# Optimization experiments

Measured on AMD Instinct MI355X. Metric: run time of the kernel, lower is better.

## Reference

```python
import jax, jax.numpy as jnp
import numpy as np
import itertools

VOXEL_SIZE = np.array([0.05, 0.05, 0.1], np.float32)   # xyz, from cfg.voxel_size
GRID_OFFSET = np.array([0.0, -40.0, -3.0], np.float32)  # xyz, cfg.grid_bounds[:3]
BN_EPS = 1e-3

# ---------------- rulebook construction (numpy, mirrors spconv indice pairs) ----------------

def _enc(c, shape):
    Z, Y, X = shape
    c = c.astype(np.int64)
    return ((c[:, 0] * Z + c[:, 1]) * Y + c[:, 2]) * X + c[:, 3]

def _lookup(sk, order, q):
    pos = np.clip(np.searchsorted(sk, q), 0, len(sk) - 1)
    return np.where((q >= 0) & (sk[pos] == q), order[pos], -1).astype(np.int32)

def _subm_rulebook(coords, shape):
    # submanifold conv k=3, pad=1: output sites == input sites; neighbor = out + (k-1)
    keys = _enc(coords, shape)
    order = np.argsort(keys).astype(np.int32)
    sk = keys[order]
    dims = np.array(shape)
    rows = []
    for off in itertools.product((-1, 0, 1), repeat=3):
        nb = coords[:, 1:] + np.array(off)
        inb = ((nb >= 0) & (nb < dims)).all(1)
        full = np.concatenate([coords[:, :1], nb], 1)
        q = np.where(inb, _enc(full, shape), -1)
        rows.append(_lookup(sk, order, q))
    return np.stack(rows)  # [27, N] input index or -1

def _strided_rulebook(coords, shape_in, ksize, stride, pad):
    # regular sparse conv: out active = any site receiving a contribution; in = out*s - p + k
    ksize = np.array(ksize); stride = np.array(stride); pad = np.array(pad)
    shape_out = tuple((((np.array(shape_in) + 2 * pad - ksize) // stride) + 1).tolist())
    keys = _enc(coords, shape_in)
    order = np.argsort(keys).astype(np.int32)
    sk = keys[order]
    cand = []
    for k in itertools.product(*[range(int(x)) for x in ksize]):
        num = coords[:, 1:] + pad - np.array(k)
        ok = (num % stride == 0).all(1)
        o = num // stride
        ok &= (o >= 0).all(1) & (o < np.array(shape_out)).all(1)
        cand.append(np.concatenate([coords[ok, :1], o[ok]], 1))
    out_coords = np.unique(np.concatenate(cand, 0), axis=0).astype(np.int32)
    dims_in = np.array(shape_in)
    rows = []
    for k in itertools.product(*[range(int(x)) for x in ksize]):
        ic = out_coords[:, 1:] * stride - pad + np.array(k)
        inb = ((ic >= 0) & (ic < dims_in)).all(1)
        full = np.concatenate([out_coords[:, :1], ic], 1)
        q = np.where(inb, _enc(full, shape_in), -1)
        rows.append(_lookup(sk, order, q))
    return out_coords, np.stack(rows), shape_out

# ---------------- inputs ----------------

def setup_inputs() -> dict:
    rng = np.random.default_rng(0)
    B, NPB = 2, 8000
    shape0 = (41, 1600, 1280)
    parts = []
    for b in range(B):
        c = np.stack([rng.integers(0, shape0[0], 4 * NPB),
                      rng.integers(0, shape0[1], 4 * NPB),
                      rng.integers(0, shape0[2], 4 * NPB)], 1)
        c = np.unique(c, axis=0)[:NPB]
        parts.append(np.concatenate([np.full((len(c), 1), b), c], 1))
    coords0 = np.concatenate(parts, 0).astype(np.int32)

    rb0 = _subm_rulebook(coords0, shape0)
    coords1, rbc1, shape1 = _strided_rulebook(coords0, shape0, (3, 3, 3), (2, 2, 2), (1, 1, 1))
    rb1 = _subm_rulebook(coords1, shape1)
    coords2, rbc2, shape2 = _strided_rulebook(coords1, shape1, (3, 3, 3), (2, 2, 2), (1, 1, 1))
    rb2 = _subm_rulebook(coords2, shape2)
    coords3, rbc3, shape3 = _strided_rulebook(coords2, shape2, (3, 3, 3), (2, 2, 2), (0, 1, 1))
    rb3 = _subm_rulebook(coords3, shape3)
    coords4, rbc4, shape4 = _strided_rulebook(coords3, shape3, (3, 1, 1), (2, 1, 1), (0, 0, 0))

    def w(*s):
        return jnp.asarray((rng.standard_normal(s) * 0.1).astype(np.float32))

    inp = {"features": jnp.asarray(rng.standard_normal((len(coords0), 4)).astype(np.float32))}
    specs = [("1a", 27, 4, 16), ("1b", 27, 16, 16), ("1c", 27, 16, 32),
             ("2a", 27, 32, 32), ("2b", 27, 32, 32), ("2c", 27, 32, 64),
             ("3a", 27, 64, 64), ("3b", 27, 64, 64), ("3c", 27, 64, 64), ("3d", 27, 64, 64),
             ("4a", 27, 64, 64), ("4b", 27, 64, 64), ("4c", 27, 64, 64), ("4d", 3, 64, 64)]
    for name, K, ci, co in specs:
        inp["w" + name] = w(K, ci, co)
        inp["g" + name] = jnp.asarray((np.abs(rng.standard_normal(co)) + 0.5).astype(np.float32))
        inp["b" + name] = jnp.asarray((rng.standard_normal(co) * 0.1).astype(np.float32))
    inp.update(coordinates=jnp.asarray(coords0), coords1=jnp.asarray(coords1),
               coords2=jnp.asarray(coords2), coords3=jnp.asarray(coords3),
               rb0=jnp.asarray(rb0), rbc1=jnp.asarray(rbc1), rb1=jnp.asarray(rb1),
               rbc2=jnp.asarray(rbc2), rb2=jnp.asarray(rb2), rbc3=jnp.asarray(rbc3),
               rb3=jnp.asarray(rb3), rbc4=jnp.asarray(rbc4), batch_size=B)
    return inp

# ---------------- forward math ----------------

def _sconv(feat, rb, W):
    # gather-GEMM-scatter: rb[k,n] = input row feeding output n via kernel offset k (-1 = none)
    out = jnp.zeros((rb.shape[1], W.shape[2]), feat.dtype)
    for k in range(W.shape[0]):
        idx = rb[k]
        g = jnp.where(idx[:, None] >= 0, feat[jnp.clip(idx, 0)], 0.0)
        out = out + g @ W[k]
    return out

def _bn_relu(x, g, b):
    # BatchNorm1d in training mode over active voxels (biased var), eps=1e-3, then ReLU
    m = jnp.mean(x, 0)
    v = jnp.mean(jnp.square(x - m), 0)
    return jax.nn.relu((x - m) * (g / jnp.sqrt(v + BN_EPS)) + b)

def reference(features, w1a, g1a, b1a, w1b, g1b, b1b, w1c, g1c, b1c,
              w2a, g2a, b2a, w2b, g2b, b2b, w2c, g2c, b2c,
              w3a, g3a, b3a, w3b, g3b, b3b, w3c, g3c, b3c, w3d, g3d, b3d,
              w4a, g4a, b4a, w4b, g4b, b4b, w4c, g4c, b4c, w4d, g4d, b4d,
              coordinates, coords1, coords2, coords3,
              rb0, rbc1, rb1, rbc2, rb2, rbc3, rb3, rbc4, batch_size):
    f0 = features
    h = _bn_relu(_sconv(f0, rb0, w1a), g1a, b1a)
    h = _bn_relu(_sconv(h, rb0, w1b), g1b, b1b)
    f1 = _bn_relu(_sconv(h, rbc1, w1c), g1c, b1c)
    h = _bn_relu(_sconv(f1, rb1, w2a), g2a, b2a)
    h = _bn_relu(_sconv(h, rb1, w2b), g2b, b2b)
    f2 = _bn_relu(_sconv(h, rbc2, w2c), g2c, b2c)
    h = _bn_relu(_sconv(f2, rb2, w3a), g3a, b3a)
    h = _bn_relu(_sconv(h, rb2, w3b), g3b, b3b)
    h = _bn_relu(_sconv(h, rb2, w3c), g3c, b3c)
    f3 = _bn_relu(_sconv(h, rbc3, w3d), g3d, b3d)
    h = _bn_relu(_sconv(f3, rb3, w4a), g4a, b4a)
    h = _bn_relu(_sconv(h, rb3, w4b), g4b, b4b)
    h = _bn_relu(_sconv(h, rb3, w4c), g4c, b4c)
    f4 = _bn_relu(_sconv(h, rbc4, w4d), g4d, b4d)

    vs = jnp.asarray(VOXEL_SIZE)
    off = jnp.asarray(GRID_OFFSET)
    def to_global(stride, c):
        # indices are (b,z,y,x); flip -> (x,y,z,b); take xyz
        return jnp.flip(c, 1)[:, :3].astype(jnp.float32) * (vs * stride) + off
    xyz0 = to_global(1, coordinates)
    xyz1 = to_global(2, coords1)
    xyz2 = to_global(4, coords2)
    xyz3 = to_global(8, coords3)
    return (xyz0, f0, xyz1, f1, xyz2, f2, xyz3, f3, f4)
```

## Files before the change

### kernel.cpp

```cpp
#include <hip/hip_runtime.h>

#define BN_EPS 1e-3f
#define NREP 16

typedef __attribute__((ext_vector_type(8))) short short8;
typedef __attribute__((ext_vector_type(4))) float float4v;

__device__ __forceinline__ short f2bf(float f) {
    unsigned u = __float_as_uint(f);
    unsigned r = (u + 0x7FFFu + ((u >> 16) & 1u)) >> 16;
    return (short)r;
}

template <int N>
__device__ __forceinline__ void waitcnt_vm() {
    __builtin_amdgcn_s_waitcnt(0xF70 | (N & 15) | ((N >> 4) << 14));
}

__device__ __forceinline__ void wave_barrier() { asm volatile("s_barrier" ::: "memory"); }

__device__ __forceinline__ void dma16(const short* g, short* l) {
    __builtin_amdgcn_global_load_lds((const __attribute__((address_space(1))) void*)g,
                                     (__attribute__((address_space(3))) void*)l, 16, 0, 0);
}


__global__ __launch_bounds__(256) void zero_kernel(float* p, int n) {
    int i = blockIdx.x * 256 + threadIdx.x;
    if (i < n) p[i] = 0.f;
}

__global__ __launch_bounds__(256) void copy_kernel(const float* __restrict__ in,
                                                   float* __restrict__ out, int n) {
    int i = blockIdx.x * 256 + threadIdx.x;
    if (i < n) out[i] = in[i];
}

__global__ __launch_bounds__(256) void zero_rows_kernel(short* a, short* b, long maxN) {
    int t = threadIdx.x;
    if (t < 32) a[maxN * 32 + t] = 0;
    else if (t < 96) a[maxN * 64 + (t - 32)] = 0;
    else if (t < 128) b[maxN * 32 + (t - 96)] = 0;
    else if (t < 192) b[maxN * 64 + (t - 128)] = 0;
}

__global__ __launch_bounds__(256) void xyz_kernel(const int* __restrict__ coords,
                                                  float* __restrict__ out, int N,
                                                  float sx, float sy, float sz) {
    int n = blockIdx.x * 256 + threadIdx.x;
    if (n >= N) return;
    int4 c = ((const int4*)coords)[n];
    out[n * 3 + 0] = c.w * sx;
    out[n * 3 + 1] = c.z * sy - 40.0f;
    out[n * 3 + 2] = c.y * sz - 3.0f;
}

__global__ __launch_bounds__(256) void convert_f0(const float* __restrict__ f,
                                                  short* __restrict__ dst, int N) {
    int i = blockIdx.x * 256 + threadIdx.x;
    if (i >= N * 32) return;
    int c = i & 31, n = i >> 5;
    dst[i] = (c < 4) ? f2bf(f[n * 4 + c]) : (short)0;
}

struct PrepAll {
    const float* src[14];
    short* dst[14];
    int CI[14];
    int CO[14];
    int CHP[14];
    int cum[15];
};

__global__ __launch_bounds__(256) void prep_all_kernel(PrepAll d) {
    int i = blockIdx.x * 256 + threadIdx.x;
    if (i >= d.cum[14]) return;
    int l = 0;
    while (l < 13 && i >= d.cum[l + 1]) ++l;
    int f = i - d.cum[l];
    int CO = d.CO[l], CI = d.CI[l];
    int NCH = d.CHP[l] / 32, CT = CO / 16;
    int e = f & 7;
    int u = f >> 3;
    int l16 = u & 15;
    int q = (u >> 4) & 3;
    int u2 = u >> 6;
    int t = u2 % CT;
    int c = (u2 / CT) % NCH;
    int k = u2 / (CT * NCH);
    int ci = c * 32 + q * 8 + e;
    int co = t * 16 + l16;
    float v = (ci < CI) ? d.src[l][((size_t)k * CI + ci) * CO + co] : 0.f;
    d.dst[l][f] = f2bf(v);
}

struct ASet {
    short8 v0, v1, v2, v3;
};

template <int CHP, int CO, int K>
__global__ __launch_bounds__(512, 4) void sconv_hyb(const short* __restrict__ feat,
                                                    const int* __restrict__ rb,
                                                    const short* __restrict__ Wt,
                                                    float* __restrict__ out,
                                                    float* __restrict__ stats, int N, int zrow) {
    constexpr int NCH = CHP / 32;
    constexpr int CT = CO / 16;
    constexpr int BTILE = CO * CHP;
    constexpr int NB = BTILE / 512;
    constexpr int A = 2 * NCH;
    constexpr int ROWS = 256;
    constexpr int WAVES = 8;
    constexpr int B0 = NB / WAVES;
    constexpr int BR = NB % WAVES;

    __shared__ __align__(16) short ldsB[3 * BTILE];
    __shared__ int sIdx[K * ROWS];
    __shared__ int sFlag[K];
    __shared__ int sKl[K];
    __shared__ int sKn;

    const int tid = threadIdx.x;
    const int w = tid >> 6;
    const int lane = tid & 63;
    const int quad = lane >> 4;
    const int l16 = lane & 15;
    const int m0 = blockIdx.x * ROWS;

    if (tid < K) sFlag[tid] = 0;
    __syncthreads();
    for (int e = tid; e < K * ROWS; e += 512) {
        int r = m0 + (e & (ROWS - 1));
        int v = (r < N) ? __builtin_nontemporal_load(&rb[(size_t)(e >> 8) * N + r]) : -1;
        sIdx[e] = v;
        if (v >= 0) sFlag[e >> 8] = 1;
    }
    __syncthreads();
    if (w == 0) {
        int f = (lane < K) ? sFlag[lane] : 0;
        unsigned long long m = __ballot(f != 0);
        if (f) sKl[__popcll(m & ((1ull << lane) - 1ull))] = lane;
        if (lane == 0) sKn = (int)__popcll(m);
    }
    __syncthreads();
    const int nk = sKn;

    const short* fquad = feat + quad * 8;

    auto issueB = [&](int kp, int slot) {
        const short* wk = Wt + (size_t)kp * BTILE + lane * 8;
        short* bb = ldsB + slot * BTILE;
#pragma unroll
        for (int jj = 0; jj < (NB + WAVES - 1) / WAVES; ++jj) {
            int j = jj * WAVES + w;
            if (j < NB) dma16(wk + j * 512, bb + j * 512);
        }
    };
    auto issueA = [&](int kp) {
        ASet s;
        int i0 = sIdx[kp * ROWS + w * 32 + l16];
        int i1 = sIdx[kp * ROWS + w * 32 + 16 + l16];
        const short* p0 = fquad + (size_t)(i0 < 0 ? zrow : i0) * CHP;
        const short* p1 = fquad + (size_t)(i1 < 0 ? zrow : i1) * CHP;
        s.v0 = *(const short8*)p0;
        s.v2 = *(const short8*)p1;
        if constexpr (NCH == 2) {
            s.v1 = *(const short8*)(p0 + 32);
            s.v3 = *(const short8*)(p1 + 32);
        } else {
            s.v1 = (short8)0;
            s.v3 = (short8)0;
        }
        return s;
    };

    float4v acc[2][CT];
#pragma unroll
    for (int mt = 0; mt < 2; ++mt)
#pragma unroll
        for (int t = 0; t < CT; ++t) acc[mt][t] = (float4v)0.f;

    ASet sA{}, sB{}, sC{};
    if (nk > 0) {
        issueB(sKl[0], 0);
        sA = issueA(sKl[0]);
    }
    if (nk > 1) {
        issueB(sKl[1], 1);
        sB = issueA(sKl[1]);
    }

    int slotRd = 0, slotWr = 2;
    for (int i = 0; i < nk; ++i) {
        if (i < nk - 1) {
            if (BR > 0 && w < BR) waitcnt_vm<B0 + 1 + A>();
            else waitcnt_vm<B0 + A>();
        } else {
            waitcnt_vm<0>();
        }
        __builtin_amdgcn_sched_barrier(0);
        wave_barrier();
        if (i + 2 < nk) {
            issueB(sKl[i + 2], slotWr);
            sC = issueA(sKl[i + 2]);
        }
        const short* bb = ldsB + slotRd * BTILE;
#pragma unroll
        for (int c = 0; c < NCH; ++c) {
#pragma unroll
            for (int t = 0; t < CT; ++t) {
                short8 bf = *(const short8*)(bb + ((c * CT + t) * 64 + quad * 16 + l16) * 8);
#pragma unroll
                for (int mt = 0; mt < 2; ++mt) {
                    short8 af = (mt == 0) ? ((c == 0) ? sA.v0 : sA.v1)
                                          : ((c == 0) ? sA.v2 : sA.v3);
                    acc[mt][t] = __builtin_amdgcn_mfma_f32_16x16x32_bf16(af, bf, acc[mt][t], 0,
                                                                         0, 0);
                }
            }
        }
        sA = sB;
        sB = sC;
        slotRd = (slotRd == 2) ? 0 : slotRd + 1;
        slotWr = (slotWr == 2) ? 0 : slotWr + 1;
    }

#pragma unroll
    for (int mt = 0; mt < 2; ++mt)
#pragma unroll
        for (int t = 0; t < CT; ++t) {
            int col = t * 16 + l16;
#pragma unroll
            for (int r = 0; r < 4; ++r) {
                int orow = m0 + w * 32 + mt * 16 + quad * 4 + r;
                if (orow < N) out[(size_t)orow * CO + col] = acc[mt][t][r];
            }
        }

    __syncthreads();
    float* red = (float*)ldsB;
#pragma unroll
    for (int t = 0; t < CT; ++t) {
        float s = 0.f, ss = 0.f;
#pragma unroll
        for (int mt = 0; mt < 2; ++mt)
#pragma unroll
            for (int r = 0; r < 4; ++r) {
                float v = acc[mt][t][r];
                s += v;
                ss += v * v;
            }
        s += __shfl_xor(s, 16);
        s += __shfl_xor(s, 32);
        ss += __shfl_xor(ss, 16);
        ss += __shfl_xor(ss, 32);
        if (lane < 16) {
            red[w * 2 * CO + t * 16 + lane] = s;
            red[w * 2 * CO + CO + t * 16 + lane] = ss;
        }
    }
    __syncthreads();
    if (tid < 2 * CO) {
        float v = 0.f;
#pragma unroll
        for (int r = 0; r < WAVES; ++r) v += red[r * 2 * CO + tid];
        float* st = stats + (size_t)(blockIdx.x & (NREP - 1)) * 128;
        atomicAdd(&st[(tid < CO) ? tid : (64 + tid - CO)], v);
    }
}

template <int COUT, int CHPN, bool F32OUT, bool BFOUT>
__global__ __launch_bounds__(256) void bn_apply(const float* __restrict__ x,
                                                const float* __restrict__ stats,
                                                const float* __restrict__ g,
                                                const float* __restrict__ b,
                                                float* __restrict__ fout,
                                                short* __restrict__ bfout, int N) {
    constexpr int CW = BFOUT ? CHPN : COUT;
    constexpr int CV = CW / 8;
    __shared__ float ssc[COUT];
    __shared__ float ssh[COUT];
    int tid = threadIdx.x;
    if (tid < COUT) {
        float s = 0.f, q = 0.f;
#pragma unroll
        for (int r = 0; r < NREP; ++r) {
            s += stats[r * 128 + tid];
            q += stats[r * 128 + 64 + tid];
        }
        float inv = 1.0f / (float)N;
        float m = s * inv;
        float v = q * inv - m * m;
        float sc = g[tid] / sqrtf(v + BN_EPS);
        ssc[tid] = sc;
        ssh[tid] = b[tid] - m * sc;
    }
    __syncthreads();
    long i = (long)blockIdx.x * 256 + tid;
    if (i >= (long)N * CV) return;
    int c8 = (int)(i % CV);
    long n = i / CV;
    int cb = c8 * 8;
    float y[8];
#pragma unroll
    for (int j = 0; j < 8; ++j) y[j] = 0.f;
    if (cb < COUT) {
        const float4v* xr = (const float4v*)(x + n * COUT + cb);
        float4v a0 = xr[0];
        float4v a1 = xr[1];
#pragma unroll
        for (int j = 0; j < 4; ++j) {
            y[j] = fmaxf(a0[j] * ssc[cb + j] + ssh[cb + j], 0.f);
            y[4 + j] = fmaxf(a1[j] * ssc[cb + 4 + j] + ssh[cb + 4 + j], 0.f);
        }
        if constexpr (F32OUT) {
            float* fo = fout + n * COUT + cb;
            if ((((unsigned long long)fout) & 15ull) == 0) {
                float4v o0, o1;
#pragma unroll
                for (int j = 0; j < 4; ++j) {
                    o0[j] = y[j];
                    o1[j] = y[4 + j];
                }
                ((float4v*)fo)[0] = o0;
                ((float4v*)fo)[1] = o1;
            } else {
#pragma unroll
                for (int j = 0; j < 8; ++j) fo[j] = y[j];
            }
        }
    }
    if constexpr (BFOUT) {
        short8 p;
#pragma unroll
        for (int j = 0; j < 8; ++j) p[j] = f2bf(y[j]);
        *(short8*)(bfout + n * CHPN + cb) = p;
    }
}


template <int CHP, int CO, int K>
static void conv(const short* fin, const int* rb, const short* wt, float* preact, float* stats,
                 int N, int zrow, hipStream_t stream) {
    dim3 grid((N + 255) / 256);
    hipLaunchKernelGGL((sconv_hyb<CHP, CO, K>), grid, dim3(512), 0, stream, fin, rb, wt, preact,
                       stats, N, zrow);
}

template <int COUT, int CHPN, bool F32OUT, bool BFOUT>
static void apply(const float* preact, const float* stats, const float* g, const float* b,
                  float* fout, short* bfout, int N, hipStream_t stream) {
    constexpr int CW = BFOUT ? CHPN : COUT;
    constexpr int CV = CW / 8;
    int blocks = (int)(((long)N * CV + 255) / 256);
    hipLaunchKernelGGL((bn_apply<COUT, CHPN, F32OUT, BFOUT>), dim3(blocks), dim3(256), 0, stream,
                       preact, stats, g, b, fout, bfout, N);
}

extern "C" void kernel_launch(void* const* d_in, const int* in_sizes, int n_in, void* d_out,
                              int out_size, void* d_ws, size_t ws_size, hipStream_t stream) {
    const float* features = (const float*)d_in[0];
    const float* W[14];
    const float* G[14];
    const float* Bb[14];
    for (int i = 0; i < 14; ++i) {
        W[i] = (const float*)d_in[1 + 3 * i];
        G[i] = (const float*)d_in[2 + 3 * i];
        Bb[i] = (const float*)d_in[3 + 3 * i];
    }
    const int* coords0 = (const int*)d_in[43];
    const int* coords1 = (const int*)d_in[44];
    const int* coords2 = (const int*)d_in[45];
    const int* coords3 = (const int*)d_in[46];
    const int* rb0 = (const int*)d_in[47];
    const int* rbc1 = (const int*)d_in[48];
    const int* rb1 = (const int*)d_in[49];
    const int* rbc2 = (const int*)d_in[50];
    const int* rb2 = (const int*)d_in[51];
    const int* rbc3 = (const int*)d_in[52];
    const int* rb3 = (const int*)d_in[53];
    const int* rbc4 = (const int*)d_in[54];

    const int N0 = in_sizes[0] / 4;
    const int N1 = in_sizes[44] / 4;
    const int N2 = in_sizes[45] / 4;
    const int N3 = in_sizes[46] / 4;
    const int N4 = in_sizes[54] / 3;

    float* out = (float*)d_out;
    long off = 0;
    float* xyz0 = out + off; off += (long)N0 * 3;
    float* f0   = out + off; off += (long)N0 * 4;
    float* xyz1 = out + off; off += (long)N1 * 3;
    float* f1   = out + off; off += (long)N1 * 32;
    float* xyz2 = out + off; off += (long)N2 * 3;
    float* f2   = out + off; off += (long)N2 * 64;
    float* xyz3 = out + off; off += (long)N3 * 3;
    float* f3   = out + off; off += (long)N3 * 64;
    float* f4   = out + off;

    long maxN = N0;
    if (N1 > maxN) maxN = N1;
    if (N2 > maxN) maxN = N2;
    if (N3 > maxN) maxN = N3;
    if (N4 > maxN) maxN = N4;
    const int zrow = (int)maxN;

    float* preact = (float*)d_ws;
    float* statsBase = preact + (size_t)maxN * 64;
    short* bfA = (short*)(statsBase + 14 * NREP * 128);
    short* bfB = bfA + (size_t)(maxN + 1) * 64;
    short* wtBase = bfB + (size_t)(maxN + 1) * 64;

    static const int KK[14] = {27, 27, 27, 27, 27, 27, 27, 27, 27, 27, 27, 27, 27, 3};
    static const int CI[14] = {4, 16, 16, 32, 32, 32, 64, 64, 64, 64, 64, 64, 64, 64};
    static const int CO[14] = {16, 16, 32, 32, 32, 64, 64, 64, 64, 64, 64, 64, 64, 64};
    short* WT[14];
    PrepAll pd;
    {
        size_t o = 0;
        int cum = 0;
        for (int l = 0; l < 14; ++l) {
            WT[l] = wtBase + o;
            int chp = CI[l] <= 32 ? 32 : 64;
            pd.src[l] = W[l];
            pd.dst[l] = WT[l];
            pd.CI[l] = CI[l];
            pd.CO[l] = CO[l];
            pd.CHP[l] = chp;
            pd.cum[l] = cum;
            cum += KK[l] * CO[l] * chp;
            o += (size_t)KK[l] * CO[l] * chp;
        }
        pd.cum[14] = cum;
    }

    int nstats = 14 * NREP * 128;
    hipLaunchKernelGGL(zero_kernel, dim3((nstats + 255) / 256), dim3(256), 0, stream, statsBase,
                       nstats);
    hipLaunchKernelGGL(zero_rows_kernel, dim3(1), dim3(256), 0, stream, bfA, bfB, maxN);
    hipLaunchKernelGGL(prep_all_kernel, dim3((pd.cum[14] + 255) / 256), dim3(256), 0, stream, pd);

    hipLaunchKernelGGL(copy_kernel, dim3((N0 * 4 + 255) / 256), dim3(256), 0, stream, features, f0,
                       N0 * 4);
    hipLaunchKernelGGL(xyz_kernel, dim3((N0 + 255) / 256), dim3(256), 0, stream, coords0, xyz0, N0,
                       0.05f, 0.05f, 0.1f);
    hipLaunchKernelGGL(xyz_kernel, dim3((N1 + 255) / 256), dim3(256), 0, stream, coords1, xyz1, N1,
                       0.1f, 0.1f, 0.2f);
    hipLaunchKernelGGL(xyz_kernel, dim3((N2 + 255) / 256), dim3(256), 0, stream, coords2, xyz2, N2,
                       0.2f, 0.2f, 0.4f);
    hipLaunchKernelGGL(xyz_kernel, dim3((N3 + 255) / 256), dim3(256), 0, stream, coords3, xyz3, N3,
                       0.4f, 0.4f, 0.8f);
    hipLaunchKernelGGL(convert_f0, dim3((N0 * 32 + 255) / 256), dim3(256), 0, stream, features,
                       bfA, N0);

    float* st = statsBase;
#define STAT(l) (st + (size_t)(l)*NREP * 128)

    conv<32, 16, 27>(bfA, rb0, WT[0], preact, STAT(0), N0, zrow, stream);
    apply<16, 32, false, true>(preact, STAT(0), G[0], Bb[0], nullptr, bfB, N0, stream);
    conv<32, 16, 27>(bfB, rb0, WT[1], preact, STAT(1), N0, zrow, stream);
    apply<16, 32, false, true>(preact, STAT(1), G[1], Bb[1], nullptr, bfA, N0, stream);
    conv<32, 32, 27>(bfA, rbc1, WT[2], preact, STAT(2), N1, zrow, stream);
    apply<32, 32, true, true>(preact, STAT(2), G[2], Bb[2], f1, bfB, N1, stream);

    conv<32, 32, 27>(bfB, rb1, WT[3], preact, STAT(3), N1, zrow, stream);
    apply<32, 32, false, true>(preact, STAT(3), G[3], Bb[3], nullptr, bfA, N1, stream);
    conv<32, 32, 27>(bfA, rb1, WT[4], preact, STAT(4), N1, zrow, stream);
    apply<32, 32, false, true>(preact, STAT(4), G[4], Bb[4], nullptr, bfB, N1, stream);
    conv<32, 64, 27>(bfB, rbc2, WT[5], preact, STAT(5), N2, zrow, stream);
    apply<64, 64, true, true>(preact, STAT(5), G[5], Bb[5], f2, bfA, N2, stream);

    conv<64, 64, 27>(bfA, rb2, WT[6], preact, STAT(6), N2, zrow, stream);
    apply<64, 64, false, true>(preact, STAT(6), G[6], Bb[6], nullptr, bfB, N2, stream);
    conv<64, 64, 27>(bfB, rb2, WT[7], preact, STAT(7), N2, zrow, stream);
    apply<64, 64, false, true>(preact, STAT(7), G[7], Bb[7], nullptr, bfA, N2, stream);
    conv<64, 64, 27>(bfA, rb2, WT[8], preact, STAT(8), N2, zrow, stream);
    apply<64, 64, false, true>(preact, STAT(8), G[8], Bb[8], nullptr, bfB, N2, stream);
    conv<64, 64, 27>(bfB, rbc3, WT[9], preact, STAT(9), N3, zrow, stream);
    apply<64, 64, true, true>(preact, STAT(9), G[9], Bb[9], f3, bfA, N3, stream);

    conv<64, 64, 27>(bfA, rb3, WT[10], preact, STAT(10), N3, zrow, stream);
    apply<64, 64, false, true>(preact, STAT(10), G[10], Bb[10], nullptr, bfB, N3, stream);
    conv<64, 64, 27>(bfB, rb3, WT[11], preact, STAT(11), N3, zrow, stream);
    apply<64, 64, false, true>(preact, STAT(11), G[11], Bb[11], nullptr, bfA, N3, stream);
    conv<64, 64, 27>(bfA, rb3, WT[12], preact, STAT(12), N3, zrow, stream);
    apply<64, 64, false, true>(preact, STAT(12), G[12], Bb[12], nullptr, bfB, N3, stream);
    conv<64, 64, 3>(bfB, rbc4, WT[13], preact, STAT(13), N4, zrow, stream);
    apply<64, 64, true, false>(preact, STAT(13), G[13], Bb[13], f4, nullptr, N4, stream);
#undef STAT
}
```

Baseline: 721.0 us.

## Stream rulebook indices per wave and shrink conv blocks to 256 threads

The sparse-conv kernel drops the LDS staging of the rulebook and the block-wide compaction of active kernel offsets. Each wave now loads its own rulebook indices directly, prefetched a few offsets ahead, and skips the MFMA work for offsets that are dead across that wave. Blocks shrink from 512 threads and 256 rows to 256 threads and 128 rows to raise occupancy and cut the startup barriers. The trade-off is that weight tiles for every offset are now always DMA'd even when the whole block has no neighbours there, and the per-wave waitcnt bookkeeping becomes more intricate.

Result: slower. 1.207 ms (+67.3%).

```diff
diff --git a/kernel.cpp b/kernel.cpp
--- a/kernel.cpp
+++ b/kernel.cpp
@@ -99,7 +99,7 @@
 };
 
 template <int CHP, int CO, int K>
-__global__ __launch_bounds__(512, 4) void sconv_hyb(const short* __restrict__ feat,
+__global__ __launch_bounds__(256, 6) void sconv_hyb(const short* __restrict__ feat,
                                                     const int* __restrict__ rb,
                                                     const short* __restrict__ Wt,
                                                     float* __restrict__ out,
@@ -109,16 +109,9 @@
     constexpr int BTILE = CO * CHP;
     constexpr int NB = BTILE / 512;
     constexpr int A = 2 * NCH;
-    constexpr int ROWS = 256;
-    constexpr int WAVES = 8;
-    constexpr int B0 = NB / WAVES;
-    constexpr int BR = NB % WAVES;
+    constexpr int ROWS = 128;
 
     __shared__ __align__(16) short ldsB[3 * BTILE];
-    __shared__ int sIdx[K * ROWS];
-    __shared__ int sFlag[K];
-    __shared__ int sKl[K];
-    __shared__ int sKn;
 
     const int tid = threadIdx.x;
     const int w = tid >> 6;
@@ -127,46 +120,44 @@
     const int l16 = lane & 15;
     const int m0 = blockIdx.x * ROWS;
 
-    if (tid < K) sFlag[tid] = 0;
-    __syncthreads();
-    for (int e = tid; e < K * ROWS; e += 512) {
-        int r = m0 + (e & (ROWS - 1));
-        int v = (r < N) ? __builtin_nontemporal_load(&rb[(size_t)(e >> 8) * N + r]) : -1;
-        sIdx[e] = v;
-        if (v >= 0) sFlag[e >> 8] = 1;
-    }
-    __syncthreads();
-    if (w == 0) {
-        int f = (lane < K) ? sFlag[lane] : 0;
-        unsigned long long m = __ballot(f != 0);
-        if (f) sKl[__popcll(m & ((1ull << lane) - 1ull))] = lane;
-        if (lane == 0) sKn = (int)__popcll(m);
-    }
-    __syncthreads();
-    const int nk = sKn;
-
     const short* fquad = feat + quad * 8;
 
+    const int r0 = m0 + (w << 5) + l16;
+    const int r1 = r0 + 16;
+    const bool v0 = r0 < N;
+    const bool v1 = r1 < N;
+    const int* p0 = rb + (v0 ? r0 : 0);
+    const int* p1 = rb + (v1 ? r1 : 0);
+
+    auto loadRb = [&](int k) {
+        int2 j;
+        j.x = p0[(size_t)k * N];
+        j.y = p1[(size_t)k * N];
+        if (!v0) j.x = -1;
+        if (!v1) j.y = -1;
+        return j;
+    };
+    auto aliveOf = [&](int2 j) {
+        return (__ballot(j.x >= 0) | __ballot(j.y >= 0)) != 0ull;
+    };
     auto issueB = [&](int kp, int slot) {
         const short* wk = Wt + (size_t)kp * BTILE + lane * 8;
         short* bb = ldsB + slot * BTILE;
 #pragma unroll
-        for (int jj = 0; jj < (NB + WAVES - 1) / WAVES; ++jj) {
-            int j = jj * WAVES + w;
+        for (int jj = 0; jj < (NB + 3) / 4; ++jj) {
+            int j = jj * 4 + w;
             if (j < NB) dma16(wk + j * 512, bb + j * 512);
         }
     };
-    auto issueA = [&](int kp) {
+    auto issueA = [&](int2 j) {
         ASet s;
-        int i0 = sIdx[kp * ROWS + w * 32 + l16];
-        int i1 = sIdx[kp * ROWS + w * 32 + 16 + l16];
-        const short* p0 = fquad + (size_t)(i0 < 0 ? zrow : i0) * CHP;
-        const short* p1 = fquad + (size_t)(i1 < 0 ? zrow : i1) * CHP;
-        s.v0 = *(const short8*)p0;
-        s.v2 = *(const short8*)p1;
+        const short* q0 = fquad + (size_t)(j.x < 0 ? zrow : j.x) * CHP;
+        const short* q1 = fquad + (size_t)(j.y < 0 ? zrow : j.y) * CHP;
+        s.v0 = *(const short8*)q0;
+        s.v2 = *(const short8*)q1;
         if constexpr (NCH == 2) {
-            s.v1 = *(const short8*)(p0 + 32);
-            s.v3 = *(const short8*)(p1 + 32);
+            s.v1 = *(const short8*)(q0 + 32);
+            s.v3 = *(const short8*)(q1 + 32);
         } else {
             s.v1 = (short8)0;
             s.v3 = (short8)0;
@@ -180,47 +171,74 @@
 #pragma unroll
         for (int t = 0; t < CT; ++t) acc[mt][t] = (float4v)0.f;
 
-    ASet sA{}, sB{}, sC{};
-    if (nk > 0) {
-        issueB(sKl[0], 0);
-        sA = issueA(sKl[0]);
-    }
-    if (nk > 1) {
-        issueB(sKl[1], 1);
-        sB = issueA(sKl[1]);
-    }
+    constexpr int BW0 = NB / 4 + ((NB % 4) > 0 ? 1 : 0);
+    constexpr int BW1 = NB / 4 + ((NB % 4) > 1 ? 1 : 0);
+    constexpr int BW2 = NB / 4 + ((NB % 4) > 2 ? 1 : 0);
+    constexpr int BW3 = NB / 4;
+
+    int2 t0 = loadRb(0);
+    int2 t1 = loadRb(1);
+    waitcnt_vm<0>();
+    bool alA = aliveOf(t0);
+    bool alB = aliveOf(t1);
+    int2 qA, qB, qC;
+    qA.x = qA.y = qB.x = qB.y = qC.x = qC.y = -1;
+    issueB(0, 0);
+    if (K > 2) qA = loadRb(2);
+    ASet sA = issueA(t0);
+    issueB(1, 1);
+    if (K > 3) qB = loadRb(3);
+    ASet sB = issueA(t1);
+    ASet sC;
+    bool alC = false;
 
     int slotRd = 0, slotWr = 2;
-    for (int i = 0; i < nk; ++i) {
-        if (i < nk - 1) {
-            if (BR > 0 && w < BR) waitcnt_vm<B0 + 1 + A>();
-            else waitcnt_vm<B0 + A>();
+#pragma unroll 1
+    for (int i = 0; i < K; ++i) {
+        if (i < K - 3) {
+            if (w == 0) waitcnt_vm<BW0 + 2 + A>();
+            else if (w == 1) waitcnt_vm<BW1 + 2 + A>();
+            else if (w == 2) waitcnt_vm<BW2 + 2 + A>();
+            else waitcnt_vm<BW3 + 2 + A>();
+        } else if (i < K - 1) {
+            if (w == 0) waitcnt_vm<BW0 + A>();
+            else if (w == 1) waitcnt_vm<BW1 + A>();
+            else if (w == 2) waitcnt_vm<BW2 + A>();
+            else waitcnt_vm<BW3 + A>();
         } else {
             waitcnt_vm<0>();
         }
         __builtin_amdgcn_sched_barrier(0);
         wave_barrier();
-        if (i + 2 < nk) {
-            issueB(sKl[i + 2], slotWr);
-            sC = issueA(sKl[i + 2]);
-        }
-        const short* bb = ldsB + slotRd * BTILE;
-#pragma unroll
-        for (int c = 0; c < NCH; ++c) {
-#pragma unroll
-            for (int t = 0; t < CT; ++t) {
-                short8 bf = *(const short8*)(bb + ((c * CT + t) * 64 + quad * 16 + l16) * 8);
-#pragma unroll
-                for (int mt = 0; mt < 2; ++mt) {
-                    short8 af = (mt == 0) ? ((c == 0) ? sA.v0 : sA.v1)
-                                          : ((c == 0) ? sA.v2 : sA.v3);
-                    acc[mt][t] = __builtin_amdgcn_mfma_f32_16x16x32_bf16(af, bf, acc[mt][t], 0,
-                                                                         0, 0);
+        if (i + 2 < K) {
+            issueB(i + 2, slotWr);
+            if (i + 4 < K) qC = loadRb(i + 4);
+            alC = aliveOf(qA);
+            sC = issueA(qA);
+        }
+        if (alA) {
+            const short* bb = ldsB + slotRd * BTILE;
+#pragma unroll
+            for (int c = 0; c < NCH; ++c) {
+#pragma unroll
+                for (int t = 0; t < CT; ++t) {
+                    short8 bf = *(const short8*)(bb + ((c * CT + t) * 64 + quad * 16 + l16) * 8);
+#pragma unroll
+                    for (int mt = 0; mt < 2; ++mt) {
+                        short8 af = (mt == 0) ? ((c == 0) ? sA.v0 : sA.v1)
+                                              : ((c == 0) ? sA.v2 : sA.v3);
+                        acc[mt][t] =
+                            __builtin_amdgcn_mfma_f32_16x16x32_bf16(af, bf, acc[mt][t], 0, 0, 0);
+                    }
                 }
             }
         }
         sA = sB;
         sB = sC;
+        alA = alB;
+        alB = alC;
+        qA = qB;
+        qB = qC;
         slotRd = (slotRd == 2) ? 0 : slotRd + 1;
         slotWr = (slotWr == 2) ? 0 : slotWr + 1;
     }
@@ -261,9 +279,7 @@
     }
     __syncthreads();
     if (tid < 2 * CO) {
-        float v = 0.f;
-#pragma unroll
-        for (int r = 0; r < WAVES; ++r) v += red[r * 2 * CO + tid];
+        float v = red[tid] + red[2 * CO + tid] + red[4 * CO + tid] + red[6 * CO + tid];
         float* st = stats + (size_t)(blockIdx.x & (NREP - 1)) * 128;
         atomicAdd(&st[(tid < CO) ? tid : (64 + tid - CO)], v);
     }
@@ -342,8 +358,8 @@
 template <int CHP, int CO, int K>
 static void conv(const short* fin, const int* rb, const short* wt, float* preact, float* stats,
                  int N, int zrow, hipStream_t stream) {
-    dim3 grid((N + 255) / 256);
-    hipLaunchKernelGGL((sconv_hyb<CHP, CO, K>), grid, dim3(512), 0, stream, fin, rb, wt, preact,
+    dim3 grid((N + 127) / 128);
+    hipLaunchKernelGGL((sconv_hyb<CHP, CO, K>), grid, dim3(256), 0, stream, fin, rb, wt, preact,
                        stats, N, zrow);
 }
 
```

## Shrink conv blocks to 128 rows and deepen weight/feature prefetch pipeline

Applied to the files above, without the earlier changes.

The sparse conv kernel moves from 512-thread blocks covering 256 rows to 256-thread blocks covering 128 rows, which doubles the grid size. The weight-tile ring in LDS grows from 3 to 6 slots, so weights are prefetched 5 offsets ahead and gathered features 3 ahead, with per-wave vmcnt waits worked out for each depth. The aim is more blocks for load balance and deeper latency hiding of the gathers and DMA. The costs are more LDS per block, which may cut occupancy, more complex wait logic, and weights being reloaded once per smaller block.

Result: slower. 748.5 us (+3.8%).

```diff
diff --git a/kernel.cpp b/kernel.cpp
--- a/kernel.cpp
+++ b/kernel.cpp
@@ -99,7 +99,7 @@
 };
 
 template <int CHP, int CO, int K>
-__global__ __launch_bounds__(512, 4) void sconv_hyb(const short* __restrict__ feat,
+__global__ __launch_bounds__(256, 3) void sconv_hyb(const short* __restrict__ feat,
                                                     const int* __restrict__ rb,
                                                     const short* __restrict__ Wt,
                                                     float* __restrict__ out,
@@ -108,13 +108,11 @@
     constexpr int CT = CO / 16;
     constexpr int BTILE = CO * CHP;
     constexpr int NB = BTILE / 512;
-    constexpr int A = 2 * NCH;
-    constexpr int ROWS = 256;
-    constexpr int WAVES = 8;
-    constexpr int B0 = NB / WAVES;
-    constexpr int BR = NB % WAVES;
-
-    __shared__ __align__(16) short ldsB[3 * BTILE];
+    constexpr int A_ = 2 * NCH;
+    constexpr int ROWS = 128;
+    constexpr int SLOTS = 6;
+
+    __shared__ __align__(16) short ldsB[SLOTS * BTILE];
     __shared__ int sIdx[K * ROWS];
     __shared__ int sFlag[K];
     __shared__ int sKl[K];
@@ -129,11 +127,11 @@
 
     if (tid < K) sFlag[tid] = 0;
     __syncthreads();
-    for (int e = tid; e < K * ROWS; e += 512) {
+    for (int e = tid; e < K * ROWS; e += 256) {
         int r = m0 + (e & (ROWS - 1));
-        int v = (r < N) ? __builtin_nontemporal_load(&rb[(size_t)(e >> 8) * N + r]) : -1;
+        int v = (r < N) ? rb[(size_t)(e >> 7) * N + r] : -1;
         sIdx[e] = v;
-        if (v >= 0) sFlag[e >> 8] = 1;
+        if (v >= 0) sFlag[e >> 7] = 1;
     }
     __syncthreads();
     if (w == 0) {
@@ -151,8 +149,8 @@
         const short* wk = Wt + (size_t)kp * BTILE + lane * 8;
         short* bb = ldsB + slot * BTILE;
 #pragma unroll
-        for (int jj = 0; jj < (NB + WAVES - 1) / WAVES; ++jj) {
-            int j = jj * WAVES + w;
+        for (int jj = 0; jj < (NB + 3) / 4; ++jj) {
+            int j = jj * 4 + w;
             if (j < NB) dma16(wk + j * 512, bb + j * 512);
         }
     };
@@ -180,29 +178,49 @@
 #pragma unroll
         for (int t = 0; t < CT; ++t) acc[mt][t] = (float4v)0.f;
 
-    ASet sA{}, sB{}, sC{};
-    if (nk > 0) {
-        issueB(sKl[0], 0);
-        sA = issueA(sKl[0]);
-    }
-    if (nk > 1) {
-        issueB(sKl[1], 1);
-        sB = issueA(sKl[1]);
-    }
-
-    int slotRd = 0, slotWr = 2;
+    constexpr int BW0 = NB / 4 + ((NB % 4) > 0 ? 1 : 0);
+    constexpr int BW1 = NB / 4 + ((NB % 4) > 1 ? 1 : 0);
+    constexpr int BW2 = NB / 4 + ((NB % 4) > 2 ? 1 : 0);
+    constexpr int BW3 = NB / 4;
+
+#define WAITW(AT, BT)                                        \
+    do {                                                     \
+        if (w == 0) waitcnt_vm<(AT)*A_ + (BT)*BW0>();        \
+        else if (w == 1) waitcnt_vm<(AT)*A_ + (BT)*BW1>();   \
+        else if (w == 2) waitcnt_vm<(AT)*A_ + (BT)*BW2>();   \
+        else waitcnt_vm<(AT)*A_ + (BT)*BW3>();               \
+    } while (0)
+
+    ASet sA{}, sB{}, sC{}, sD{};
+#pragma unroll
+    for (int s = 0; s < 5; ++s)
+        if (s < nk) issueB(sKl[s], s);
+    if (nk > 0) sA = issueA(sKl[0]);
+    if (nk > 1) sB = issueA(sKl[1]);
+    if (nk > 2) sC = issueA(sKl[2]);
+
+    int slotRd = 0, slotWr = 5;
+#pragma unroll 1
     for (int i = 0; i < nk; ++i) {
-        if (i < nk - 1) {
-            if (BR > 0 && w < BR) waitcnt_vm<B0 + 1 + A>();
-            else waitcnt_vm<B0 + A>();
+        if (i + 3 < nk) sD = issueA(sKl[i + 3]);
+        const int d = nk - 1 - i;
+        if (i >= 3) {
+            if (d >= 4) WAITW(3, 3);
+            else if (d == 3) WAITW(3, 2);
+            else if (d == 2) WAITW(2, 1);
+            else if (d == 1) WAITW(1, 0);
+            else WAITW(0, 0);
         } else {
-            waitcnt_vm<0>();
+            if (d >= 3) WAITW(3, 0);
+            else if (d == 2) WAITW(2, 0);
+            else if (d == 1) WAITW(1, 0);
+            else WAITW(0, 0);
         }
         __builtin_amdgcn_sched_barrier(0);
         wave_barrier();
-        if (i + 2 < nk) {
-            issueB(sKl[i + 2], slotWr);
-            sC = issueA(sKl[i + 2]);
+        if (i + 5 < nk) {
+            issueB(sKl[i + 5], slotWr);
+            slotWr = (slotWr == SLOTS - 1) ? 0 : slotWr + 1;
         }
         const short* bb = ldsB + slotRd * BTILE;
 #pragma unroll
@@ -221,9 +239,10 @@
         }
         sA = sB;
         sB = sC;
-        slotRd = (slotRd == 2) ? 0 : slotRd + 1;
-        slotWr = (slotWr == 2) ? 0 : slotWr + 1;
-    }
+        sC = sD;
+        slotRd = (slotRd == SLOTS - 1) ? 0 : slotRd + 1;
+    }
+#undef WAITW
 
 #pragma unroll
     for (int mt = 0; mt < 2; ++mt)
@@ -261,9 +280,7 @@
     }
     __syncthreads();
     if (tid < 2 * CO) {
-        float v = 0.f;
-#pragma unroll
-        for (int r = 0; r < WAVES; ++r) v += red[r * 2 * CO + tid];
+        float v = red[tid] + red[2 * CO + tid] + red[4 * CO + tid] + red[6 * CO + tid];
         float* st = stats + (size_t)(blockIdx.x & (NREP - 1)) * 128;
         atomicAdd(&st[(tid < CO) ? tid : (64 + tid - CO)], v);
     }
@@ -342,8 +359,8 @@
 template <int CHP, int CO, int K>
 static void conv(const short* fin, const int* rb, const short* wt, float* preact, float* stats,
                  int N, int zrow, hipStream_t stream) {
-    dim3 grid((N + 255) / 256);
-    hipLaunchKernelGGL((sconv_hyb<CHP, CO, K>), grid, dim3(512), 0, stream, fin, rb, wt, preact,
+    dim3 grid((N + 127) / 128);
+    hipLaunchKernelGGL((sconv_hyb<CHP, CO, K>), grid, dim3(256), 0, stream, fin, rb, wt, preact,
                        stats, N, zrow);
 }
 
```
